# Optimization experiments

Measured on AMD Instinct MI355X. Metric: run time of the kernel, lower is better.

Reference implementation:

```python
import jax, jax.numpy as jnp
import numpy as np

B, S, H = 32, 1024, 512
NEG = -1e10

def setup_inputs() -> dict:
    key = jax.random.key(0)
    k1, k2, k3, k4, k5, k6 = jax.random.split(key, 6)
    return {
        "hidden": jax.random.normal(k1, (B, H), jnp.float32),
        "encoder_outputs": jax.random.normal(k2, (B, S, 2 * H), jnp.float32),
        "mask": jax.random.randint(k3, (B, S), 0, 2, jnp.int32),
        "W_attn": jax.random.normal(k4, (3 * H, H), jnp.float32) * (1.0 / np.sqrt(3 * H)),
        "b_attn": jax.random.normal(k5, (H,), jnp.float32) * 0.01,
        "W_v": jax.random.normal(k6, (H,), jnp.float32) * (1.0 / np.sqrt(H)),
    }

def reference(hidden, encoder_outputs, mask, W_attn, b_attn, W_v):
    # Split the concat-matmul: cat([h, enc]) @ W_attn == h @ W_h + enc @ W_e
    W_h, W_e = W_attn[:H], W_attn[H:]            # [H,H], [2H,H]
    proj_h = hidden @ W_h                        # [B, H]
    proj_e = jnp.einsum('bse,eh->bsh', encoder_outputs, W_e)  # [B, S, H]
    energy = jnp.tanh(proj_h[:, None, :] + proj_e + b_attn)   # [B, S, H]
    scores = jnp.einsum('bsh,h->bs', energy, W_v)             # [B, S]
    scores = jnp.where(mask == 0, NEG, scores)
    attn_w = jax.nn.softmax(scores, axis=1)                   # [B, S]
    context = jnp.einsum('bs,bse->be', attn_w, encoder_outputs)  # [B, 2H]
    return context, attn_w
```

## Files before the change

### kernel.cpp

```cpp
#include <hip/hip_runtime.h>
#include <hip/hip_bf16.h>
#include <math.h>

#define NB 32
#define NS 1024
#define NH 512
#define NE 1024
#define NEGV -1e10f

typedef _Float16 f16x8 __attribute__((ext_vector_type(8)));
typedef _Float16 f16x4 __attribute__((ext_vector_type(4)));
typedef float f32x4 __attribute__((ext_vector_type(4)));

__device__ __forceinline__ float fast_tanh(float x) {
  float t = __expf(2.f * x);
  return (t - 1.f) * __builtin_amdgcn_rcpf(t + 1.f);
}

__global__ __launch_bounds__(256) void proj_h_kernel(
    const float* __restrict__ hidden, const float* __restrict__ W_attn,
    const float* __restrict__ b_attn, float* __restrict__ c) {
  int b = blockIdx.x >> 1;
  int h = ((blockIdx.x & 1) << 8) + threadIdx.x;
  __shared__ float hid[NH];
  for (int e = threadIdx.x; e < NH; e += 256) hid[e] = hidden[b * NH + e];
  __syncthreads();
  float acc = b_attn[h];
#pragma unroll 8
  for (int e = 0; e < NH; ++e) acc = fmaf(hid[e], W_attn[(size_t)e * NH + h], acc);
  c[b * NH + h] = acc;
}

__global__ __launch_bounds__(256) void prep_We_kernel(
    const float* __restrict__ W_attn, _Float16* __restrict__ WeT) {
  int k = blockIdx.x;
  const float* src = W_attn + (size_t)(NH + k) * NH;
#pragma unroll
  for (int j = 0; j < 2; ++j) {
    int col = threadIdx.x + (j << 8);
    WeT[(size_t)col * NE + k] = (_Float16)src[col];
  }
}

__global__ __launch_bounds__(512) void score_kernel(
    const float* __restrict__ enc, const _Float16* __restrict__ WeT,
    const float* __restrict__ c, const float* __restrict__ Wv,
    float* __restrict__ spart) {
  __shared__ float Asm[2][128 * 64];
  __shared__ _Float16 Bsm[2][256 * 64];
  const int tid = threadIdx.x;
  const int lane = tid & 63;
  const int wid = tid >> 6;
  const int wr = wid >> 2;
  const int wc = wid & 3;
  const int r15 = lane & 15;
  const int id = blockIdx.x;
  const int lb = ((id & 7) << 6) + (id >> 3);
  const int mt = lb >> 1;
  const int nc = lb & 1;
  const int b = mt >> 3;
  const int s0 = (mt & 7) << 7;
  const char* Abase = (const char*)(enc + ((size_t)b * NS + s0) * NE);
  const char* Wbase = (const char*)(WeT + ((size_t)(nc << 8)) * NE);

  f32x4 acc[4][4];
#pragma unroll
  for (int i = 0; i < 4; ++i)
#pragma unroll
    for (int j = 0; j < 4; ++j) acc[i][j] = (f32x4)0.f;

#define STAGE(KT, BUF)                                                           \
  {                                                                              \
    _Pragma("unroll") for (int i = 0; i < 4; ++i) {                              \
      int dbase = (i << 13) + (wid << 10);                                       \
      int d = dbase + (lane << 4);                                               \
      int row = d >> 8;                                                          \
      int sb = (d & 255) ^ ((row & 15) << 4);                                    \
      __builtin_amdgcn_global_load_lds(                                          \
          (const __attribute__((address_space(1))) uint32_t*)(Abase + (size_t)row * 4096 + ((KT) << 8) + sb), \
          (__attribute__((address_space(3))) uint32_t*)((char*)Asm[BUF] + dbase),\
          16, 0, 0);                                                             \
    }                                                                            \
    _Pragma("unroll") for (int i = 0; i < 4; ++i) {                              \
      int dbase = (i << 13) + (wid << 10);                                       \
      int d = dbase + (lane << 4);                                               \
      int col = d >> 7;                                                          \
      int sb = (d & 127) ^ ((col & 7) << 4);                                     \
      __builtin_amdgcn_global_load_lds(                                          \
          (const __attribute__((address_space(1))) uint32_t*)(Wbase + (size_t)col * 2048 + ((KT) << 7) + sb), \
          (__attribute__((address_space(3))) uint32_t*)((char*)Bsm[BUF] + dbase),\
          16, 0, 0);                                                             \
    }                                                                            \
  }

#define COMPUTE(CUR)                                                             \
  _Pragma("unroll") for (int kk = 0; kk < 2; ++kk) {                             \
    f16x8 af[4], bf[4];                                                          \
    _Pragma("unroll") for (int mi = 0; mi < 4; ++mi) {                           \
      int row = (wr << 6) + (mi << 4) + r15;                                     \
      int off1 = (row << 8) + (kk << 7) + ((lane >> 4) << 5);                    \
      int x = (row & 15) << 4;                                                   \
      f32x4 u = *(const f32x4*)((const char*)Asm[CUR] + (off1 ^ x));             \
      f32x4 v = *(const f32x4*)((const char*)Asm[CUR] + ((off1 + 16) ^ x));      \
      f16x8 h;                                                                   \
      h[0] = (_Float16)u[0]; h[1] = (_Float16)u[1];                              \
      h[2] = (_Float16)u[2]; h[3] = (_Float16)u[3];                              \
      h[4] = (_Float16)v[0]; h[5] = (_Float16)v[1];                              \
      h[6] = (_Float16)v[2]; h[7] = (_Float16)v[3];                              \
      af[mi] = h;                                                                \
    }                                                                            \
    _Pragma("unroll") for (int nj = 0; nj < 4; ++nj) {                           \
      int cb = (wc << 6) + (nj << 4) + r15;                                      \
      int off = (cb << 7) + (kk << 6) + ((lane >> 4) << 4);                      \
      off ^= (cb & 7) << 4;                                                      \
      bf[nj] = *(const f16x8*)((const char*)Bsm[CUR] + off);                     \
    }                                                                            \
    _Pragma("unroll") for (int mi = 0; mi < 4; ++mi)                             \
      _Pragma("unroll") for (int nj = 0; nj < 4; ++nj)                           \
        acc[mi][nj] = __builtin_amdgcn_mfma_f32_16x16x32_f16(af[mi], bf[nj],     \
                                                             acc[mi][nj], 0, 0, 0); \
  }

  STAGE(0, 0);
  asm volatile("s_waitcnt vmcnt(0)" ::: "memory");
  __builtin_amdgcn_s_barrier();
  __builtin_amdgcn_sched_barrier(0);

  for (int kt = 0; kt < 15; ++kt) {
    const int cur = kt & 1, nxt = cur ^ 1;
    STAGE(kt + 1, nxt);
    asm volatile("s_waitcnt vmcnt(8)" ::: "memory");
    __builtin_amdgcn_s_barrier();
    __builtin_amdgcn_sched_barrier(0);
    COMPUTE(cur);
    asm volatile("s_waitcnt lgkmcnt(0)" ::: "memory");
    __builtin_amdgcn_s_barrier();
    __builtin_amdgcn_sched_barrier(0);
  }
  asm volatile("s_waitcnt vmcnt(0)" ::: "memory");
  __builtin_amdgcn_s_barrier();
  __builtin_amdgcn_sched_barrier(0);
  COMPUTE(1);
#undef STAGE
#undef COMPUTE

  float sr[4][4];
#pragma unroll
  for (int i = 0; i < 4; ++i)
#pragma unroll
    for (int r = 0; r < 4; ++r) sr[i][r] = 0.f;
#pragma unroll
  for (int nj = 0; nj < 4; ++nj) {
    int hcol = (nc << 8) + (wc << 6) + (nj << 4) + r15;
    float wvj = Wv[hcol];
    float cvj = c[b * NH + hcol];
#pragma unroll
    for (int mi = 0; mi < 4; ++mi)
#pragma unroll
      for (int r = 0; r < 4; ++r)
        sr[mi][r] += wvj * fast_tanh(acc[mi][nj][r] + cvj);
  }
#pragma unroll
  for (int off = 1; off < 16; off <<= 1)
#pragma unroll
    for (int mi = 0; mi < 4; ++mi)
#pragma unroll
      for (int r = 0; r < 4; ++r) sr[mi][r] += __shfl_xor(sr[mi][r], off, 64);
  if (r15 == 0) {
    float* dst = spart + (size_t)((nc << 2) + wc) * NB * NS + b * NS + s0 + (wr << 6);
#pragma unroll
    for (int mi = 0; mi < 4; ++mi)
#pragma unroll
      for (int r = 0; r < 4; ++r)
        dst[(mi << 4) + ((lane >> 4) << 2) + r] = sr[mi][r];
  }
}

__global__ __launch_bounds__(256) void softmax_kernel(
    const float* __restrict__ spart, const int* __restrict__ mask,
    float* __restrict__ attn) {
  int b = blockIdx.x, tid = threadIdx.x;
  __shared__ float red[8];
  float v[4];
  float mx = -INFINITY;
#pragma unroll
  for (int j = 0; j < 4; ++j) {
    int s = tid + (j << 8);
    float x = 0.f;
#pragma unroll
    for (int p = 0; p < 8; ++p) x += spart[(size_t)p * NB * NS + b * NS + s];
    v[j] = (mask[b * NS + s] == 0) ? NEGV : x;
    mx = fmaxf(mx, v[j]);
  }
#pragma unroll
  for (int off = 32; off >= 1; off >>= 1) mx = fmaxf(mx, __shfl_xor(mx, off, 64));
  if ((tid & 63) == 0) red[tid >> 6] = mx;
  __syncthreads();
  mx = fmaxf(fmaxf(red[0], red[1]), fmaxf(red[2], red[3]));
  float sum = 0.f;
#pragma unroll
  for (int j = 0; j < 4; ++j) {
    v[j] = __expf(v[j] - mx);
    sum += v[j];
  }
#pragma unroll
  for (int off = 32; off >= 1; off >>= 1) sum += __shfl_xor(sum, off, 64);
  __syncthreads();
  if ((tid & 63) == 0) red[4 + (tid >> 6)] = sum;
  __syncthreads();
  float inv = 1.f / (red[4] + red[5] + red[6] + red[7]);
#pragma unroll
  for (int j = 0; j < 4; ++j) attn[b * NS + tid + (j << 8)] = v[j] * inv;
}

__global__ __launch_bounds__(256) void ctx_partial_kernel(
    const float* __restrict__ enc, const float* __restrict__ attn,
    float* __restrict__ partial) {
  int ch = blockIdx.x;
  int b = blockIdx.y;
  int tid = threadIdx.x;
  __shared__ float w[64];
  if (tid < 64) w[tid] = attn[b * NS + (ch << 6) + tid];
  __syncthreads();
  const float* encb = enc + ((size_t)b * NS + (ch << 6)) * NE;
  float4 acc = make_float4(0.f, 0.f, 0.f, 0.f);
  int e = tid << 2;
  for (int s = 0; s < 64; ++s) {
    float4 x = *(const float4*)(encb + (size_t)s * NE + e);
    float ws_ = w[s];
    acc.x = fmaf(ws_, x.x, acc.x);
    acc.y = fmaf(ws_, x.y, acc.y);
    acc.z = fmaf(ws_, x.z, acc.z);
    acc.w = fmaf(ws_, x.w, acc.w);
  }
  *(float4*)(partial + ((size_t)(b * 16 + ch)) * NE + e) = acc;
}

__global__ __launch_bounds__(256) void ctx_reduce_kernel(
    const float* __restrict__ partial, float* __restrict__ ctx) {
  int b = blockIdx.x;
  int e = threadIdx.x << 2;
  float4 acc = make_float4(0.f, 0.f, 0.f, 0.f);
  for (int ch = 0; ch < 16; ++ch) {
    float4 x = *(const float4*)(partial + ((size_t)(b * 16 + ch)) * NE + e);
    acc.x += x.x;
    acc.y += x.y;
    acc.z += x.z;
    acc.w += x.w;
  }
  *(float4*)(ctx + (size_t)b * NE + e) = acc;
}

extern "C" void kernel_launch(void* const* d_in, const int* in_sizes, int n_in,
                              void* d_out, int out_size, void* d_ws, size_t ws_size,
                              hipStream_t stream) {
  const float* hidden = (const float*)d_in[0];
  const float* enc = (const float*)d_in[1];
  const int* mask = (const int*)d_in[2];
  const float* W_attn = (const float*)d_in[3];
  const float* b_attn = (const float*)d_in[4];
  const float* W_v = (const float*)d_in[5];

  float* ctx = (float*)d_out;
  float* attn = ctx + NB * NS;

  char* ws = (char*)d_ws;
  float* c = (float*)ws;
  float* spart = (float*)(ws + 65536);
  float* partial = (float*)(ws + 65536 + 1048576);
  _Float16* WeT = (_Float16*)(ws + 65536 + 1048576 + 2097152);

  proj_h_kernel<<<64, 256, 0, stream>>>(hidden, W_attn, b_attn, c);
  prep_We_kernel<<<NE, 256, 0, stream>>>(W_attn, WeT);
  score_kernel<<<512, 512, 0, stream>>>(enc, WeT, c, W_v, spart);
  softmax_kernel<<<NB, 256, 0, stream>>>(spart, mask, attn);
  ctx_partial_kernel<<<dim3(16, NB), 256, 0, stream>>>(enc, attn, partial);
  ctx_reduce_kernel<<<NB, 256, 0, stream>>>(partial, ctx);
}
```

Measured before the change: 119.9 us.

## Retile score GEMM to full-H 64-row tiles and reduce scores in-block

The score GEMM changes from 128x256 output tiles with K-step 64 to 64x512 tiles (all of H) with K-step 32. This lets each block finish the tanh/W_v reduction in LDS and write final scores directly, so the 8-way partial-score buffer and its summation in softmax go away. LDS per block shrinks and occupancy is hinted at 4 blocks per CU. In exchange, the hand-tuned waitcnt/barrier pipeline is replaced with plain __syncthreads and twice as many K iterations, and the fp16 W_e tile is now reloaded by every row block with less reuse per byte.

```diff
diff --git a/kernel.cpp b/kernel.cpp
--- a/kernel.cpp
+++ b/kernel.cpp
@@ -42,26 +42,21 @@
   }
 }
 
-__global__ __launch_bounds__(512) void score_kernel(
+__global__ __launch_bounds__(512, 4) void score_kernel(
     const float* __restrict__ enc, const _Float16* __restrict__ WeT,
     const float* __restrict__ c, const float* __restrict__ Wv,
-    float* __restrict__ spart) {
-  __shared__ float Asm[2][128 * 64];
-  __shared__ _Float16 Bsm[2][256 * 64];
+    float* __restrict__ scores) {
+  __shared__ float Asm[2][64 * 32];
+  __shared__ _Float16 Bsm[2][512 * 32];
   const int tid = threadIdx.x;
   const int lane = tid & 63;
   const int wid = tid >> 6;
-  const int wr = wid >> 2;
-  const int wc = wid & 3;
   const int r15 = lane & 15;
-  const int id = blockIdx.x;
-  const int lb = ((id & 7) << 6) + (id >> 3);
-  const int mt = lb >> 1;
-  const int nc = lb & 1;
-  const int b = mt >> 3;
-  const int s0 = (mt & 7) << 7;
+  const int mt = blockIdx.x;
+  const int b = mt >> 4;
+  const int s0 = (mt & 15) << 6;
   const char* Abase = (const char*)(enc + ((size_t)b * NS + s0) * NE);
-  const char* Wbase = (const char*)(WeT + ((size_t)(nc << 8)) * NE);
+  const char* Wbase = (const char*)WeT;
 
   f32x4 acc[4][4];
 #pragma unroll
@@ -71,35 +66,33 @@
 
 #define STAGE(KT, BUF)                                                           \
   {                                                                              \
+    {                                                                            \
+      int d = tid << 4;                                                          \
+      int row = d >> 7;                                                          \
+      int sb = (d & 127) ^ ((row & 7) << 4);                                     \
+      __builtin_amdgcn_global_load_lds(                                          \
+          (const __attribute__((address_space(1))) uint32_t*)(Abase + (size_t)row * 4096 + ((KT) << 7) + sb), \
+          (__attribute__((address_space(3))) uint32_t*)((char*)Asm[BUF] + (wid << 10)), \
+          16, 0, 0);                                                             \
+    }                                                                            \
     _Pragma("unroll") for (int i = 0; i < 4; ++i) {                              \
-      int dbase = (i << 13) + (wid << 10);                                       \
-      int d = dbase + (lane << 4);                                               \
-      int row = d >> 8;                                                          \
-      int sb = (d & 255) ^ ((row & 15) << 4);                                    \
+      int d = (i << 13) + (tid << 4);                                            \
+      int col = d >> 6;                                                          \
+      int sb = (d & 63) ^ (((col >> 1) & 3) << 4);                               \
       __builtin_amdgcn_global_load_lds(                                          \
-          (const __attribute__((address_space(1))) uint32_t*)(Abase + (size_t)row * 4096 + ((KT) << 8) + sb), \
-          (__attribute__((address_space(3))) uint32_t*)((char*)Asm[BUF] + dbase),\
+          (const __attribute__((address_space(1))) uint32_t*)(Wbase + (size_t)col * 2048 + ((KT) << 6) + sb), \
+          (__attribute__((address_space(3))) uint32_t*)((char*)Bsm[BUF] + (i << 13) + (wid << 10)), \
           16, 0, 0);                                                             \
     }                                                                            \
-    _Pragma("unroll") for (int i = 0; i < 4; ++i) {                              \
-      int dbase = (i << 13) + (wid << 10);                                       \
-      int d = dbase + (lane << 4);                                               \
-      int col = d >> 7;                                                          \
-      int sb = (d & 127) ^ ((col & 7) << 4);                                     \
-      __builtin_amdgcn_global_load_lds(                                          \
-          (const __attribute__((address_space(1))) uint32_t*)(Wbase + (size_t)col * 2048 + ((KT) << 7) + sb), \
-          (__attribute__((address_space(3))) uint32_t*)((char*)Bsm[BUF] + dbase),\
-          16, 0, 0);                                                             \
-    }                                                                            \
   }
 
 #define COMPUTE(CUR)                                                             \
-  _Pragma("unroll") for (int kk = 0; kk < 2; ++kk) {                             \
+  {                                                                              \
     f16x8 af[4], bf[4];                                                          \
     _Pragma("unroll") for (int mi = 0; mi < 4; ++mi) {                           \
-      int row = (wr << 6) + (mi << 4) + r15;                                     \
-      int off1 = (row << 8) + (kk << 7) + ((lane >> 4) << 5);                    \
-      int x = (row & 15) << 4;                                                   \
+      int row = (mi << 4) + r15;                                                 \
+      int off1 = (row << 7) + ((lane >> 4) << 5);                                \
+      int x = (row & 7) << 4;                                                    \
       f32x4 u = *(const f32x4*)((const char*)Asm[CUR] + (off1 ^ x));             \
       f32x4 v = *(const f32x4*)((const char*)Asm[CUR] + ((off1 + 16) ^ x));      \
       f16x8 h;                                                                   \
@@ -110,9 +103,9 @@
       af[mi] = h;                                                                \
     }                                                                            \
     _Pragma("unroll") for (int nj = 0; nj < 4; ++nj) {                           \
-      int cb = (wc << 6) + (nj << 4) + r15;                                      \
-      int off = (cb << 7) + (kk << 6) + ((lane >> 4) << 4);                      \
-      off ^= (cb & 7) << 4;                                                      \
+      int col = (wid << 6) + (nj << 4) + r15;                                    \
+      int off = (col << 6) + ((lane >> 4) << 4);                                 \
+      off ^= ((col >> 1) & 3) << 4;                                              \
       bf[nj] = *(const f16x8*)((const char*)Bsm[CUR] + off);                     \
     }                                                                            \
     _Pragma("unroll") for (int mi = 0; mi < 4; ++mi)                             \
@@ -122,25 +115,13 @@
   }
 
   STAGE(0, 0);
-  asm volatile("s_waitcnt vmcnt(0)" ::: "memory");
-  __builtin_amdgcn_s_barrier();
-  __builtin_amdgcn_sched_barrier(0);
-
-  for (int kt = 0; kt < 15; ++kt) {
+  __syncthreads();
+  for (int kt = 0; kt < 32; ++kt) {
     const int cur = kt & 1, nxt = cur ^ 1;
-    STAGE(kt + 1, nxt);
-    asm volatile("s_waitcnt vmcnt(8)" ::: "memory");
-    __builtin_amdgcn_s_barrier();
-    __builtin_amdgcn_sched_barrier(0);
+    if (kt < 31) STAGE(kt + 1, nxt);
     COMPUTE(cur);
-    asm volatile("s_waitcnt lgkmcnt(0)" ::: "memory");
-    __builtin_amdgcn_s_barrier();
-    __builtin_amdgcn_sched_barrier(0);
-  }
-  asm volatile("s_waitcnt vmcnt(0)" ::: "memory");
-  __builtin_amdgcn_s_barrier();
-  __builtin_amdgcn_sched_barrier(0);
-  COMPUTE(1);
+    __syncthreads();
+  }
 #undef STAGE
 #undef COMPUTE
 
@@ -151,7 +132,7 @@
     for (int r = 0; r < 4; ++r) sr[i][r] = 0.f;
 #pragma unroll
   for (int nj = 0; nj < 4; ++nj) {
-    int hcol = (nc << 8) + (wc << 6) + (nj << 4) + r15;
+    int hcol = (wid << 6) + (nj << 4) + r15;
     float wvj = Wv[hcol];
     float cvj = c[b * NH + hcol];
 #pragma unroll
@@ -166,18 +147,25 @@
     for (int mi = 0; mi < 4; ++mi)
 #pragma unroll
       for (int r = 0; r < 4; ++r) sr[mi][r] += __shfl_xor(sr[mi][r], off, 64);
+  float* red = (float*)Asm;
   if (r15 == 0) {
-    float* dst = spart + (size_t)((nc << 2) + wc) * NB * NS + b * NS + s0 + (wr << 6);
 #pragma unroll
     for (int mi = 0; mi < 4; ++mi)
 #pragma unroll
       for (int r = 0; r < 4; ++r)
-        dst[(mi << 4) + ((lane >> 4) << 2) + r] = sr[mi][r];
+        red[(wid << 6) + (mi << 4) + ((lane >> 4) << 2) + r] = sr[mi][r];
+  }
+  __syncthreads();
+  if (tid < 64) {
+    float s = 0.f;
+#pragma unroll
+    for (int w = 0; w < 8; ++w) s += red[(w << 6) + tid];
+    scores[b * NS + s0 + tid] = s;
   }
 }
 
 __global__ __launch_bounds__(256) void softmax_kernel(
-    const float* __restrict__ spart, const int* __restrict__ mask,
+    const float* __restrict__ scores, const int* __restrict__ mask,
     float* __restrict__ attn) {
   int b = blockIdx.x, tid = threadIdx.x;
   __shared__ float red[8];
@@ -186,9 +174,7 @@
 #pragma unroll
   for (int j = 0; j < 4; ++j) {
     int s = tid + (j << 8);
-    float x = 0.f;
-#pragma unroll
-    for (int p = 0; p < 8; ++p) x += spart[(size_t)p * NB * NS + b * NS + s];
+    float x = scores[b * NS + s];
     v[j] = (mask[b * NS + s] == 0) ? NEGV : x;
     mx = fmaxf(mx, v[j]);
   }
@@ -266,14 +252,14 @@
 
   char* ws = (char*)d_ws;
   float* c = (float*)ws;
-  float* spart = (float*)(ws + 65536);
-  float* partial = (float*)(ws + 65536 + 1048576);
-  _Float16* WeT = (_Float16*)(ws + 65536 + 1048576 + 2097152);
+  float* scores = (float*)(ws + 65536);
+  float* partial = (float*)(ws + 65536 + 131072);
+  _Float16* WeT = (_Float16*)(ws + 65536 + 131072 + 2097152);
 
   proj_h_kernel<<<64, 256, 0, stream>>>(hidden, W_attn, b_attn, c);
   prep_We_kernel<<<NE, 256, 0, stream>>>(W_attn, WeT);
-  score_kernel<<<512, 512, 0, stream>>>(enc, WeT, c, W_v, spart);
-  softmax_kernel<<<NB, 256, 0, stream>>>(spart, mask, attn);
+  score_kernel<<<512, 512, 0, stream>>>(enc, WeT, c, W_v, scores);
+  softmax_kernel<<<NB, 256, 0, stream>>>(scores, mask, attn);
   ctx_partial_kernel<<<dim3(16, NB), 256, 0, stream>>>(enc, attn, partial);
   ctx_reduce_kernel<<<NB, 256, 0, stream>>>(partial, ctx);
 }
```

New measurement: 115.8 us. -3.4%, faster.

## Drop double-buffered LDS staging in score kernel to fit two blocks per CU

Applied to the files above, without the earlier changes.

Replaces the double-buffered A/B shared-memory tiles with single buffers and a simple load, sync, compute, sync loop over the 16 K-tiles. This halves LDS use per block from about 128KB to 64KB, so two 512-thread blocks can be resident per CU and the 512-block grid can run in one wave instead of two. In exchange, each block no longer overlaps its next tile's global-to-LDS loads with MFMA compute. It now relies on the other resident block to hide that latency.

```diff
diff --git a/kernel.cpp b/kernel.cpp
--- a/kernel.cpp
+++ b/kernel.cpp
@@ -46,8 +46,8 @@
     const float* __restrict__ enc, const _Float16* __restrict__ WeT,
     const float* __restrict__ c, const float* __restrict__ Wv,
     float* __restrict__ spart) {
-  __shared__ float Asm[2][128 * 64];
-  __shared__ _Float16 Bsm[2][256 * 64];
+  __shared__ float Asm[128 * 64];
+  __shared__ _Float16 Bsm[256 * 64];
   const int tid = threadIdx.x;
   const int lane = tid & 63;
   const int wid = tid >> 6;
@@ -69,7 +69,7 @@
 #pragma unroll
     for (int j = 0; j < 4; ++j) acc[i][j] = (f32x4)0.f;
 
-#define STAGE(KT, BUF)                                                           \
+#define STAGE(KT)                                                                \
   {                                                                              \
     _Pragma("unroll") for (int i = 0; i < 4; ++i) {                              \
       int dbase = (i << 13) + (wid << 10);                                       \
@@ -78,7 +78,7 @@
       int sb = (d & 255) ^ ((row & 15) << 4);                                    \
       __builtin_amdgcn_global_load_lds(                                          \
           (const __attribute__((address_space(1))) uint32_t*)(Abase + (size_t)row * 4096 + ((KT) << 8) + sb), \
-          (__attribute__((address_space(3))) uint32_t*)((char*)Asm[BUF] + dbase),\
+          (__attribute__((address_space(3))) uint32_t*)((char*)Asm + dbase),     \
           16, 0, 0);                                                             \
     }                                                                            \
     _Pragma("unroll") for (int i = 0; i < 4; ++i) {                              \
@@ -88,20 +88,20 @@
       int sb = (d & 127) ^ ((col & 7) << 4);                                     \
       __builtin_amdgcn_global_load_lds(                                          \
           (const __attribute__((address_space(1))) uint32_t*)(Wbase + (size_t)col * 2048 + ((KT) << 7) + sb), \
-          (__attribute__((address_space(3))) uint32_t*)((char*)Bsm[BUF] + dbase),\
+          (__attribute__((address_space(3))) uint32_t*)((char*)Bsm + dbase),     \
           16, 0, 0);                                                             \
     }                                                                            \
   }
 
-#define COMPUTE(CUR)                                                             \
+#define COMPUTE()                                                                \
   _Pragma("unroll") for (int kk = 0; kk < 2; ++kk) {                             \
     f16x8 af[4], bf[4];                                                          \
     _Pragma("unroll") for (int mi = 0; mi < 4; ++mi) {                           \
       int row = (wr << 6) + (mi << 4) + r15;                                     \
       int off1 = (row << 8) + (kk << 7) + ((lane >> 4) << 5);                    \
       int x = (row & 15) << 4;                                                   \
-      f32x4 u = *(const f32x4*)((const char*)Asm[CUR] + (off1 ^ x));             \
-      f32x4 v = *(const f32x4*)((const char*)Asm[CUR] + ((off1 + 16) ^ x));      \
+      f32x4 u = *(const f32x4*)((const char*)Asm + (off1 ^ x));                  \
+      f32x4 v = *(const f32x4*)((const char*)Asm + ((off1 + 16) ^ x));           \
       f16x8 h;                                                                   \
       h[0] = (_Float16)u[0]; h[1] = (_Float16)u[1];                              \
       h[2] = (_Float16)u[2]; h[3] = (_Float16)u[3];                              \
@@ -113,7 +113,7 @@
       int cb = (wc << 6) + (nj << 4) + r15;                                      \
       int off = (cb << 7) + (kk << 6) + ((lane >> 4) << 4);                      \
       off ^= (cb & 7) << 4;                                                      \
-      bf[nj] = *(const f16x8*)((const char*)Bsm[CUR] + off);                     \
+      bf[nj] = *(const f16x8*)((const char*)Bsm + off);                          \
     }                                                                            \
     _Pragma("unroll") for (int mi = 0; mi < 4; ++mi)                             \
       _Pragma("unroll") for (int nj = 0; nj < 4; ++nj)                           \
@@ -121,26 +121,12 @@
                                                              acc[mi][nj], 0, 0, 0); \
   }
 
-  STAGE(0, 0);
-  asm volatile("s_waitcnt vmcnt(0)" ::: "memory");
-  __builtin_amdgcn_s_barrier();
-  __builtin_amdgcn_sched_barrier(0);
-
-  for (int kt = 0; kt < 15; ++kt) {
-    const int cur = kt & 1, nxt = cur ^ 1;
-    STAGE(kt + 1, nxt);
-    asm volatile("s_waitcnt vmcnt(8)" ::: "memory");
-    __builtin_amdgcn_s_barrier();
-    __builtin_amdgcn_sched_barrier(0);
-    COMPUTE(cur);
-    asm volatile("s_waitcnt lgkmcnt(0)" ::: "memory");
-    __builtin_amdgcn_s_barrier();
-    __builtin_amdgcn_sched_barrier(0);
-  }
-  asm volatile("s_waitcnt vmcnt(0)" ::: "memory");
-  __builtin_amdgcn_s_barrier();
-  __builtin_amdgcn_sched_barrier(0);
-  COMPUTE(1);
+  for (int kt = 0; kt < 16; ++kt) {
+    STAGE(kt);
+    __syncthreads();
+    COMPUTE();
+    __syncthreads();
+  }
 #undef STAGE
 #undef COMPUTE
 
```

New measurement: 122.2 us. Within noise of the previous version (+1.9%).
